# Performance work log

Hardware: AMD Instinct MI355X
Metric: run time of the kernel (lower is better)

Reference implementation:

```python
import jax, jax.numpy as jnp
import numpy as np

ALPHA = 0.2  # LeakyReLU negative slope


def setup_inputs() -> dict:
    key = jax.random.key(0)
    k1, k2, k3, k4 = jax.random.split(key, 4)
    B, N, D_in, D_out = 8, 2048, 128, 128
    h = jax.random.normal(k1, (B, N, D_in), dtype=jnp.float32)
    adj = jax.random.randint(k2, (B, N, N), 0, 2, dtype=jnp.int32)
    # params: W maps D_in->D_out (Linear, no bias); a maps 2*D_out->1 (no bias)
    W = jax.random.normal(k3, (D_in, D_out), dtype=jnp.float32) / np.sqrt(D_in)
    a = jax.random.normal(k4, (2 * D_out,), dtype=jnp.float32) / np.sqrt(2 * D_out)
    return {"h": h, "adj": adj, "W": W, "a": a}


def reference(h, adj, W, a):
    # h: (B,N,D_in), adj: (B,N,N) int, W: (D_in,D_out), a: (2*D_out,)
    D_out = W.shape[1]
    Wh = jnp.einsum("bnd,de->bne", h, W)  # (B,N,D_out)
    # a^T [Wh_i ; Wh_j] decomposes as a_src.Wh_i + a_dst.Wh_j -> avoids (B,N,N,2D) concat
    a_src, a_dst = a[:D_out], a[D_out:]
    s_i = Wh @ a_src  # (B,N) score contribution of row node i
    s_j = Wh @ a_dst  # (B,N) score contribution of col node j
    e = jax.nn.leaky_relu(s_i[:, :, None] + s_j[:, None, :], negative_slope=ALPHA)  # (B,N,N)
    e = jnp.where(adj == 0, -jnp.inf, e)
    attention = jax.nn.softmax(e, axis=-1)  # (B,N,N)
    h_prime = jnp.einsum("bij,bjd->bid", attention, Wh)  # (B,N,D_out)
    return h_prime
```

## Files before the change

### kernel.cpp

```cpp
#include <hip/hip_runtime.h>
#include <hip/hip_bf16.h>

typedef __bf16 bf16x8 __attribute__((ext_vector_type(8)));
typedef __bf16 bf16x4 __attribute__((ext_vector_type(4)));
typedef float  f32x4  __attribute__((ext_vector_type(4)));
typedef float  flt4v  __attribute__((ext_vector_type(4)));
typedef int    int4v  __attribute__((ext_vector_type(4)));

#define ALPHA 0.2f
#define LOG2E 1.44269504089f

__global__ __launch_bounds__(256) void gat_wh(
    const float* __restrict__ h,
    const float* __restrict__ W,
    const float* __restrict__ a,
    __bf16* __restrict__ T,
    float* __restrict__ ssrc,
    float* __restrict__ sdst)
{
    __shared__ __bf16 Wt[128][136];
    __shared__ float wvs[128], wvd[128];
    const int tid = threadIdx.x;
    if (tid < 128) {
        float s0 = 0.f, s1 = 0.f;
        const float* wr = W + tid * 128;
        #pragma unroll 4
        for (int e = 0; e < 128; ++e) {
            float w = wr[e];
            s0 += w * a[e];
            s1 += w * a[128 + e];
        }
        wvs[tid] = s0; wvd[tid] = s1;
    }
    #pragma unroll
    for (int it = 0; it < 8; ++it) {
        int o = (it * 256 + tid) * 8;
        flt4v v0 = *reinterpret_cast<const flt4v*>(W + o);
        flt4v v1 = *reinterpret_cast<const flt4v*>(W + o + 4);
        int d = o >> 7, e = o & 127;
        #pragma unroll
        for (int j = 0; j < 4; ++j) {
            Wt[e + j][d]     = (__bf16)v0[j];
            Wt[e + 4 + j][d] = (__bf16)v1[j];
        }
    }
    __syncthreads();
    const int wave = tid >> 6, lane = tid & 63;
    const int lr = lane & 15, lg = lane >> 4;
    const int row0 = blockIdx.x * 64 + wave * 16;
    f32x4 acc[8];
    #pragma unroll
    for (int ct = 0; ct < 8; ++ct) acc[ct] = (f32x4){0.f, 0.f, 0.f, 0.f};
    #pragma unroll
    for (int kk = 0; kk < 4; ++kk) {
        const float* hp = h + (size_t)(row0 + lr) * 128 + kk * 32 + lg * 8;
        flt4v h0 = *reinterpret_cast<const flt4v*>(hp);
        flt4v h1 = *reinterpret_cast<const flt4v*>(hp + 4);
        bf16x8 af;
        #pragma unroll
        for (int j = 0; j < 4; ++j) { af[j] = (__bf16)h0[j]; af[4 + j] = (__bf16)h1[j]; }
        #pragma unroll
        for (int ct = 0; ct < 8; ++ct) {
            bf16x8 bf_ = *reinterpret_cast<const bf16x8*>(&Wt[ct * 16 + lr][kk * 32 + lg * 8]);
            acc[ct] = __builtin_amdgcn_mfma_f32_16x16x32_bf16(af, bf_, acc[ct], 0, 0, 0);
        }
    }
    const int b  = row0 >> 11;
    const int n0 = row0 & 2047;
    __bf16* tb = T + (size_t)b * 262144;
    const int j0t = n0 + lg * 4;
    const int jt  = j0t >> 6;
    const int kk2 = (j0t >> 5) & 1;
    const int lgp = (j0t >> 3) & 3;
    const int u0  = j0t & 7;
    #pragma unroll
    for (int ct = 0; ct < 8; ++ct) {
        bf16x4 v;
        #pragma unroll
        for (int q = 0; q < 4; ++q) v[q] = (__bf16)acc[ct][q];
        *reinterpret_cast<bf16x4*>(tb + ((jt * 2 + kk2) * 8 + ct) * 512 + lgp * 128 + lr * 8 + u0) = v;
    }
    const float* hrow = h + (size_t)(row0 + lr) * 128 + lg * 32;
    float s0 = 0.f, s1 = 0.f;
    #pragma unroll
    for (int u = 0; u < 32; u += 4) {
        flt4v hv = *reinterpret_cast<const flt4v*>(hrow + u);
        #pragma unroll
        for (int q = 0; q < 4; ++q) {
            float x = hv[q];
            s0 += x * wvs[lg * 32 + u + q];
            s1 += x * wvd[lg * 32 + u + q];
        }
    }
    s0 += __shfl_xor(s0, 16, 64); s0 += __shfl_xor(s0, 32, 64);
    s1 += __shfl_xor(s1, 16, 64); s1 += __shfl_xor(s1, 32, 64);
    if (lg == 0) {
        ssrc[row0 + lr] = s0 * LOG2E;
        sdst[row0 + lr] = s1 * LOG2E;
    }
}

__global__ __launch_bounds__(512) void gat_attn(
    const int* __restrict__ adj,
    const __bf16* __restrict__ T,
    const float* __restrict__ ssrc,
    const float* __restrict__ sdst,
    float* __restrict__ out)
{
    __shared__ __bf16 Pl[2][8][512];
    __shared__ float  lsumf[32];
    __shared__ f32x4  mbuf[4][2][2][64];

    const int tid = threadIdx.x, w = tid >> 6, l = tid & 63;
    const int lr = l & 15, lg = l >> 4;
    const int kkR = w >> 2, cp = w & 3;
    const int b  = blockIdx.x & 7;
    const int i0 = (blockIdx.x >> 3) << 5;

    const int prow = 4 * w + (l >> 4);
    const int row  = i0 + prow;
    const int jc   = (l & 15) * 8;
    const int pt2  = (l & 15) >> 3;
    const int pkk  = ((l & 15) >> 2) & 1;
    const int plgp = (l & 15) & 3;
    const int pbuf = pt2 * 4 + (w >> 2) * 2 + pkk;
    const int pslot = (prow & 15) + plgp * 16;
    const float si = ssrc[b * 2048 + row];
    const int* arow = adj + ((size_t)b * 2048 + row) * 2048;
    const float* sd = sdst + b * 2048;
    const __bf16* tb = T + (size_t)b * 262144;

    f32x4 acc[2][2];
    #pragma unroll
    for (int g = 0; g < 2; ++g)
        #pragma unroll
        for (int c2 = 0; c2 < 2; ++c2) acc[g][c2] = (f32x4){0.f, 0.f, 0.f, 0.f};
    float lrow = 0.f;

    {
        int4v a0 = *reinterpret_cast<const int4v*>(arow + jc);
        int4v a1 = *reinterpret_cast<const int4v*>(arow + jc + 4);
        flt4v s0 = *reinterpret_cast<const flt4v*>(sd + jc);
        flt4v s1 = *reinterpret_cast<const flt4v*>(sd + jc + 4);
        bf16x8 pw;
        #pragma unroll
        for (int u = 0; u < 4; ++u) {
            float e0 = si + s0[u], e1 = si + s1[u];
            e0 = fmaxf(e0, ALPHA * e0); e1 = fmaxf(e1, ALPHA * e1);
            float p0 = exp2f(e0), p1 = exp2f(e1);
            p0 = (a0[u] != 0) ? p0 : 0.f;
            p1 = (a1[u] != 0) ? p1 : 0.f;
            __bf16 pb0 = (__bf16)p0, pb1 = (__bf16)p1;
            lrow += (float)pb0 + (float)pb1;
            pw[u] = pb0; pw[4 + u] = pb1;
        }
        *reinterpret_cast<bf16x8*>(&Pl[0][pbuf][pslot * 8]) = pw;
    }
    __syncthreads();

    #pragma unroll 2
    for (int iv = 0; iv < 16; ++iv) {
        const int cur = iv & 1, nxt = cur ^ 1;
        const int jt0 = iv * 2;
        int4v an0 = {0,0,0,0}, an1 = {0,0,0,0};
        flt4v sn0, sn1;
        if (iv < 15) {
            const int off = (iv + 1) * 128 + jc;
            an0 = *reinterpret_cast<const int4v*>(arow + off);
            an1 = *reinterpret_cast<const int4v*>(arow + off + 4);
            sn0 = *reinterpret_cast<const flt4v*>(sd + off);
            sn1 = *reinterpret_cast<const flt4v*>(sd + off + 4);
        }
        const __bf16* tk0 = tb + (size_t)(((jt0 * 2 + kkR) * 8) + cp * 2) * 512 + l * 8;
        const __bf16* tk1 = tb + (size_t)((((jt0 + 1) * 2 + kkR) * 8) + cp * 2) * 512 + l * 8;
        bf16x8 b00 = *reinterpret_cast<const bf16x8*>(tk0);
        bf16x8 b01 = *reinterpret_cast<const bf16x8*>(tk0 + 512);
        bf16x8 b10 = *reinterpret_cast<const bf16x8*>(tk1);
        bf16x8 b11 = *reinterpret_cast<const bf16x8*>(tk1 + 512);
        bf16x8 a00 = *reinterpret_cast<const bf16x8*>(&Pl[cur][0 + 0 + kkR][l * 8]);
        bf16x8 a01 = *reinterpret_cast<const bf16x8*>(&Pl[cur][0 + 2 + kkR][l * 8]);
        bf16x8 a10 = *reinterpret_cast<const bf16x8*>(&Pl[cur][4 + 0 + kkR][l * 8]);
        bf16x8 a11 = *reinterpret_cast<const bf16x8*>(&Pl[cur][4 + 2 + kkR][l * 8]);
        acc[0][0] = __builtin_amdgcn_mfma_f32_16x16x32_bf16(a00, b00, acc[0][0], 0, 0, 0);
        acc[0][1] = __builtin_amdgcn_mfma_f32_16x16x32_bf16(a00, b01, acc[0][1], 0, 0, 0);
        acc[1][0] = __builtin_amdgcn_mfma_f32_16x16x32_bf16(a01, b00, acc[1][0], 0, 0, 0);
        acc[1][1] = __builtin_amdgcn_mfma_f32_16x16x32_bf16(a01, b01, acc[1][1], 0, 0, 0);
        acc[0][0] = __builtin_amdgcn_mfma_f32_16x16x32_bf16(a10, b10, acc[0][0], 0, 0, 0);
        acc[0][1] = __builtin_amdgcn_mfma_f32_16x16x32_bf16(a10, b11, acc[0][1], 0, 0, 0);
        acc[1][0] = __builtin_amdgcn_mfma_f32_16x16x32_bf16(a11, b10, acc[1][0], 0, 0, 0);
        acc[1][1] = __builtin_amdgcn_mfma_f32_16x16x32_bf16(a11, b11, acc[1][1], 0, 0, 0);
        if (iv < 15) {
            bf16x8 pw;
            #pragma unroll
            for (int u = 0; u < 4; ++u) {
                float e0 = si + sn0[u], e1 = si + sn1[u];
                e0 = fmaxf(e0, ALPHA * e0); e1 = fmaxf(e1, ALPHA * e1);
                float p0 = exp2f(e0), p1 = exp2f(e1);
                p0 = (an0[u] != 0) ? p0 : 0.f;
                p1 = (an1[u] != 0) ? p1 : 0.f;
                __bf16 pb0 = (__bf16)p0, pb1 = (__bf16)p1;
                lrow += (float)pb0 + (float)pb1;
                pw[u] = pb0; pw[4 + u] = pb1;
            }
            *reinterpret_cast<bf16x8*>(&Pl[nxt][pbuf][pslot * 8]) = pw;
        }
        __syncthreads();
    }

    lrow += __shfl_xor(lrow, 1, 64);
    lrow += __shfl_xor(lrow, 2, 64);
    lrow += __shfl_xor(lrow, 4, 64);
    lrow += __shfl_xor(lrow, 8, 64);
    if ((l & 15) == 0) lsumf[prow] = lrow;
    if (kkR == 1) {
        #pragma unroll
        for (int g = 0; g < 2; ++g)
            #pragma unroll
            for (int c2 = 0; c2 < 2; ++c2)
                mbuf[cp][g][c2][l] = acc[g][c2];
    }
    __syncthreads();
    if (kkR == 0) {
        #pragma unroll
        for (int g = 0; g < 2; ++g) {
            float den[4];
            #pragma unroll
            for (int q = 0; q < 4; ++q) den[q] = lsumf[g * 16 + lg * 4 + q];
            #pragma unroll
            for (int c2 = 0; c2 < 2; ++c2) {
                f32x4 av = acc[g][c2];
                f32x4 mv = mbuf[cp][g][c2][l];
                const int col = (cp * 2 + c2) * 16 + lr;
                #pragma unroll
                for (int q = 0; q < 4; ++q) {
                    const int orow = i0 + g * 16 + lg * 4 + q;
                    out[((size_t)b * 2048 + orow) * 128 + col] = (av[q] + mv[q]) / den[q];
                }
            }
        }
    }
}

extern "C" void kernel_launch(void* const* d_in, const int* in_sizes, int n_in,
                              void* d_out, int out_size, void* d_ws, size_t ws_size,
                              hipStream_t stream)
{
    const float* h = nullptr; const int* adj = nullptr;
    const float* W = nullptr; const float* a = nullptr;
    for (int i = 0; i < n_in; ++i) {
        switch (in_sizes[i]) {
            case 2097152:  h   = (const float*)d_in[i]; break;
            case 33554432: adj = (const int*)d_in[i];   break;
            case 16384:    W   = (const float*)d_in[i]; break;
            case 256:      a   = (const float*)d_in[i]; break;
        }
    }
    if (!h || !adj || !W || !a) {
        h   = (const float*)d_in[0];
        adj = (const int*)d_in[1];
        W   = (const float*)d_in[2];
        a   = (const float*)d_in[3];
    }

    __bf16* T = (__bf16*)d_ws;
    float* ssrc = (float*)((char*)d_ws + (size_t)4 * 1024 * 1024);
    float* sdst = ssrc + 8 * 2048;

    gat_wh<<<256, 256, 0, stream>>>(h, W, a, T, ssrc, sdst);
    gat_attn<<<512, 512, 0, stream>>>(adj, T, ssrc, sdst, (float*)d_out);
}
```

Baseline: 46.66 us.

## Halve rows per attention block and split K across waves with shared-memory reduction

The attention kernel now handles 16 query rows per block instead of 32 and launches twice as many blocks. The eight waves split the work by column tile and K half, each running four MFMAs per iteration on one shared P fragment. Partial sums are then combined through a serialized shared-memory accumulation and written out with vectorized stores. The aim is more parallelism and better latency hiding on the adj stream, at the cost of reading each T tile twice as many times across blocks and adding a four-step reduction with extra barriers.

```diff
diff --git a/kernel.cpp b/kernel.cpp
--- a/kernel.cpp
+++ b/kernel.cpp
@@ -107,102 +107,85 @@
     const float* __restrict__ sdst,
     float* __restrict__ out)
 {
-    __shared__ __bf16 Pl[2][8][512];
-    __shared__ float  lsumf[32];
-    __shared__ f32x4  mbuf[4][2][2][64];
+    __shared__ __bf16 Pl[2][4][512];
+    __shared__ float accsh[16][132];
+    __shared__ float lsumf[16];
 
     const int tid = threadIdx.x, w = tid >> 6, l = tid & 63;
-    const int lr = l & 15, lg = l >> 4;
-    const int kkR = w >> 2, cp = w & 3;
     const int b  = blockIdx.x & 7;
-    const int i0 = (blockIdx.x >> 3) << 5;
-
-    const int prow = 4 * w + (l >> 4);
+    const int i0 = (blockIdx.x >> 3) << 4;
+
+    const int prow = 2 * w + (l >> 5);
     const int row  = i0 + prow;
-    const int jc   = (l & 15) * 8;
-    const int pt2  = (l & 15) >> 3;
-    const int pkk  = ((l & 15) >> 2) & 1;
-    const int plgp = (l & 15) & 3;
-    const int pbuf = pt2 * 4 + (w >> 2) * 2 + pkk;
-    const int pslot = (prow & 15) + plgp * 16;
+    const int l5   = l & 31;
+    const int jc   = l5 * 4;
+    const int pbuf  = (l5 >> 4) * 2 + ((l5 >> 3) & 1);
+    const int palane = prow + ((l5 & 7) >> 1) * 16;
+    const int pu0   = (l5 & 1) * 4;
     const float si = ssrc[b * 2048 + row];
     const int* arow = adj + ((size_t)b * 2048 + row) * 2048;
     const float* sd = sdst + b * 2048;
     const __bf16* tb = T + (size_t)b * 262144;
 
-    f32x4 acc[2][2];
-    #pragma unroll
-    for (int g = 0; g < 2; ++g)
-        #pragma unroll
-        for (int c2 = 0; c2 < 2; ++c2) acc[g][c2] = (f32x4){0.f, 0.f, 0.f, 0.f};
+    const int t2w = w >> 2, kkw = (w >> 1) & 1, cp = w & 1;
+
+    f32x4 acc[4];
+    #pragma unroll
+    for (int c = 0; c < 4; ++c) acc[c] = (f32x4){0.f, 0.f, 0.f, 0.f};
     float lrow = 0.f;
 
     {
         int4v a0 = *reinterpret_cast<const int4v*>(arow + jc);
-        int4v a1 = *reinterpret_cast<const int4v*>(arow + jc + 4);
         flt4v s0 = *reinterpret_cast<const flt4v*>(sd + jc);
-        flt4v s1 = *reinterpret_cast<const flt4v*>(sd + jc + 4);
-        bf16x8 pw;
+        bf16x4 pw;
         #pragma unroll
         for (int u = 0; u < 4; ++u) {
-            float e0 = si + s0[u], e1 = si + s1[u];
-            e0 = fmaxf(e0, ALPHA * e0); e1 = fmaxf(e1, ALPHA * e1);
-            float p0 = exp2f(e0), p1 = exp2f(e1);
-            p0 = (a0[u] != 0) ? p0 : 0.f;
-            p1 = (a1[u] != 0) ? p1 : 0.f;
-            __bf16 pb0 = (__bf16)p0, pb1 = (__bf16)p1;
-            lrow += (float)pb0 + (float)pb1;
-            pw[u] = pb0; pw[4 + u] = pb1;
-        }
-        *reinterpret_cast<bf16x8*>(&Pl[0][pbuf][pslot * 8]) = pw;
+            float e = si + s0[u];
+            e = fmaxf(e, ALPHA * e);
+            float p = exp2f(e);
+            p = (a0[u] != 0) ? p : 0.f;
+            __bf16 pb = (__bf16)p;
+            lrow += (float)pb;
+            pw[u] = pb;
+        }
+        *reinterpret_cast<bf16x4*>(&Pl[0][pbuf][palane * 8 + pu0]) = pw;
     }
     __syncthreads();
 
     #pragma unroll 2
     for (int iv = 0; iv < 16; ++iv) {
         const int cur = iv & 1, nxt = cur ^ 1;
-        const int jt0 = iv * 2;
-        int4v an0 = {0,0,0,0}, an1 = {0,0,0,0};
-        flt4v sn0, sn1;
+        const int jt = iv * 2 + t2w;
+        int4v an = {0, 0, 0, 0};
+        flt4v sn;
         if (iv < 15) {
             const int off = (iv + 1) * 128 + jc;
-            an0 = *reinterpret_cast<const int4v*>(arow + off);
-            an1 = *reinterpret_cast<const int4v*>(arow + off + 4);
-            sn0 = *reinterpret_cast<const flt4v*>(sd + off);
-            sn1 = *reinterpret_cast<const flt4v*>(sd + off + 4);
-        }
-        const __bf16* tk0 = tb + (size_t)(((jt0 * 2 + kkR) * 8) + cp * 2) * 512 + l * 8;
-        const __bf16* tk1 = tb + (size_t)((((jt0 + 1) * 2 + kkR) * 8) + cp * 2) * 512 + l * 8;
-        bf16x8 b00 = *reinterpret_cast<const bf16x8*>(tk0);
-        bf16x8 b01 = *reinterpret_cast<const bf16x8*>(tk0 + 512);
-        bf16x8 b10 = *reinterpret_cast<const bf16x8*>(tk1);
-        bf16x8 b11 = *reinterpret_cast<const bf16x8*>(tk1 + 512);
-        bf16x8 a00 = *reinterpret_cast<const bf16x8*>(&Pl[cur][0 + 0 + kkR][l * 8]);
-        bf16x8 a01 = *reinterpret_cast<const bf16x8*>(&Pl[cur][0 + 2 + kkR][l * 8]);
-        bf16x8 a10 = *reinterpret_cast<const bf16x8*>(&Pl[cur][4 + 0 + kkR][l * 8]);
-        bf16x8 a11 = *reinterpret_cast<const bf16x8*>(&Pl[cur][4 + 2 + kkR][l * 8]);
-        acc[0][0] = __builtin_amdgcn_mfma_f32_16x16x32_bf16(a00, b00, acc[0][0], 0, 0, 0);
-        acc[0][1] = __builtin_amdgcn_mfma_f32_16x16x32_bf16(a00, b01, acc[0][1], 0, 0, 0);
-        acc[1][0] = __builtin_amdgcn_mfma_f32_16x16x32_bf16(a01, b00, acc[1][0], 0, 0, 0);
-        acc[1][1] = __builtin_amdgcn_mfma_f32_16x16x32_bf16(a01, b01, acc[1][1], 0, 0, 0);
-        acc[0][0] = __builtin_amdgcn_mfma_f32_16x16x32_bf16(a10, b10, acc[0][0], 0, 0, 0);
-        acc[0][1] = __builtin_amdgcn_mfma_f32_16x16x32_bf16(a10, b11, acc[0][1], 0, 0, 0);
-        acc[1][0] = __builtin_amdgcn_mfma_f32_16x16x32_bf16(a11, b10, acc[1][0], 0, 0, 0);
-        acc[1][1] = __builtin_amdgcn_mfma_f32_16x16x32_bf16(a11, b11, acc[1][1], 0, 0, 0);
+            an = *reinterpret_cast<const int4v*>(arow + off);
+            sn = *reinterpret_cast<const flt4v*>(sd + off);
+        }
+        const __bf16* tk = tb + (size_t)(((jt * 2 + kkw) * 8) + cp * 4) * 512 + l * 8;
+        bf16x8 bf0 = *reinterpret_cast<const bf16x8*>(tk);
+        bf16x8 bf1 = *reinterpret_cast<const bf16x8*>(tk + 512);
+        bf16x8 bf2 = *reinterpret_cast<const bf16x8*>(tk + 1024);
+        bf16x8 bf3 = *reinterpret_cast<const bf16x8*>(tk + 1536);
+        bf16x8 af = *reinterpret_cast<const bf16x8*>(&Pl[cur][t2w * 2 + kkw][l * 8]);
+        acc[0] = __builtin_amdgcn_mfma_f32_16x16x32_bf16(af, bf0, acc[0], 0, 0, 0);
+        acc[1] = __builtin_amdgcn_mfma_f32_16x16x32_bf16(af, bf1, acc[1], 0, 0, 0);
+        acc[2] = __builtin_amdgcn_mfma_f32_16x16x32_bf16(af, bf2, acc[2], 0, 0, 0);
+        acc[3] = __builtin_amdgcn_mfma_f32_16x16x32_bf16(af, bf3, acc[3], 0, 0, 0);
         if (iv < 15) {
-            bf16x8 pw;
+            bf16x4 pw;
             #pragma unroll
             for (int u = 0; u < 4; ++u) {
-                float e0 = si + sn0[u], e1 = si + sn1[u];
-                e0 = fmaxf(e0, ALPHA * e0); e1 = fmaxf(e1, ALPHA * e1);
-                float p0 = exp2f(e0), p1 = exp2f(e1);
-                p0 = (an0[u] != 0) ? p0 : 0.f;
-                p1 = (an1[u] != 0) ? p1 : 0.f;
-                __bf16 pb0 = (__bf16)p0, pb1 = (__bf16)p1;
-                lrow += (float)pb0 + (float)pb1;
-                pw[u] = pb0; pw[4 + u] = pb1;
+                float e = si + sn[u];
+                e = fmaxf(e, ALPHA * e);
+                float p = exp2f(e);
+                p = (an[u] != 0) ? p : 0.f;
+                __bf16 pb = (__bf16)p;
+                lrow += (float)pb;
+                pw[u] = pb;
             }
-            *reinterpret_cast<bf16x8*>(&Pl[nxt][pbuf][pslot * 8]) = pw;
+            *reinterpret_cast<bf16x4*>(&Pl[nxt][pbuf][palane * 8 + pu0]) = pw;
         }
         __syncthreads();
     }
@@ -211,34 +194,33 @@
     lrow += __shfl_xor(lrow, 2, 64);
     lrow += __shfl_xor(lrow, 4, 64);
     lrow += __shfl_xor(lrow, 8, 64);
-    if ((l & 15) == 0) lsumf[prow] = lrow;
-    if (kkR == 1) {
-        #pragma unroll
-        for (int g = 0; g < 2; ++g)
+    lrow += __shfl_xor(lrow, 16, 64);
+    if (l5 == 0) lsumf[prow] = lrow;
+
+    #pragma unroll
+    for (int s = 0; s < 4; ++s) {
+        if ((w >> 1) == s) {
             #pragma unroll
-            for (int c2 = 0; c2 < 2; ++c2)
-                mbuf[cp][g][c2][l] = acc[g][c2];
-    }
-    __syncthreads();
-    if (kkR == 0) {
-        #pragma unroll
-        for (int g = 0; g < 2; ++g) {
-            float den[4];
-            #pragma unroll
-            for (int q = 0; q < 4; ++q) den[q] = lsumf[g * 16 + lg * 4 + q];
-            #pragma unroll
-            for (int c2 = 0; c2 < 2; ++c2) {
-                f32x4 av = acc[g][c2];
-                f32x4 mv = mbuf[cp][g][c2][l];
-                const int col = (cp * 2 + c2) * 16 + lr;
+            for (int c = 0; c < 4; ++c) {
+                const int col = (cp * 4 + c) * 16 + (l & 15);
                 #pragma unroll
                 for (int q = 0; q < 4; ++q) {
-                    const int orow = i0 + g * 16 + lg * 4 + q;
-                    out[((size_t)b * 2048 + orow) * 128 + col] = (av[q] + mv[q]) / den[q];
+                    const int r = (l >> 4) * 4 + q;
+                    if (s == 0) accsh[r][col] = acc[c][q];
+                    else        accsh[r][col] += acc[c][q];
                 }
             }
         }
-    }
+        __syncthreads();
+    }
+
+    const int r  = tid >> 5;
+    const int c0 = (tid & 31) * 4;
+    const float den = lsumf[r];
+    flt4v o;
+    #pragma unroll
+    for (int u = 0; u < 4; ++u) o[u] = accsh[r][c0 + u] / den;
+    *reinterpret_cast<flt4v*>(out + ((size_t)b * 2048 + i0 + r) * 128 + c0) = o;
 }
 
 extern "C" void kernel_launch(void* const* d_in, const int* in_sizes, int n_in,
@@ -267,5 +249,5 @@
     float* sdst = ssrc + 8 * 2048;
 
     gat_wh<<<256, 256, 0, stream>>>(h, W, a, T, ssrc, sdst);
-    gat_attn<<<512, 512, 0, stream>>>(adj, T, ssrc, sdst, (float*)d_out);
+    gat_attn<<<1024, 512, 0, stream>>>(adj, T, ssrc, sdst, (float*)d_out);
 }
```

New measurement: 56.52 us. 1.21x slower.
